# Kernel optimization log

Measured on AMD Instinct MI355X. Metric: run time of the kernel, lower is better.

The kernel has to match this reference:

```python
import jax, jax.numpy as jnp
import numpy as np

N = 4096; E = 65536; IN = 512; H = 256; QD = 256; NH = 8; HD = QD // NH
OUT = 10; L = 2; CT = 50


def _ln(x, g, b, eps=1e-5):
    mu = x.mean(-1, keepdims=True)
    var = ((x - mu) ** 2).mean(-1, keepdims=True)
    return (x - mu) * jax.lax.rsqrt(var + eps) * g + b


def _forward(x, edge_index, cell_types, Wi, bi, Wq, bq, Wk, bk, Wv, bv, Bc, cemb,
             Win, bin_p, Wo, bo, Wm1, bm1, Wm2, bm2, Wm3, bm3, ln_g, ln_b,
             Wc1, bc1, Wc2, bc2):
    src, tgt = edge_index[0], edge_index[1]
    h = jax.nn.relu(x @ Wi + bi)                      # [N, H] input projection
    # graph connectivity scattered into a dense mask (as in _create_attention_mask)
    mask = jnp.zeros((N, N), jnp.float32).at[src, tgt].set(1.0)
    for l in range(L):
        res = h
        Q = h @ Wq[l] + bq[l]                         # [N, QD]
        K = h @ Wk[l] + bk[l]
        V = h @ Wv[l] + bv[l]
        Q = Q @ Bc[l]                                 # biological constraint
        K = K @ Bc[l].T
        ce = cemb[l][cell_types]                      # [N, QD] cell-type embedding
        Q = Q + 0.1 * ce
        K = K + 0.1 * ce
        # dense graph-masked attention (entanglement matrix), applied to V
        scores = (Q @ K.T) / float(np.sqrt(QD))      # [N, N]
        scores = jnp.where(mask == 0.0, -1e9, scores)
        attn = jax.nn.softmax(scores, axis=-1)
        graph_att = attn @ V                          # [N, QD]
        # nn.MultiheadAttention(Q, K, V) entanglement layer (eval mode)
        q = (Q @ Win[l, :, :QD] + bin_p[l, :QD]).reshape(N, NH, HD)
        k = (K @ Win[l, :, QD:2 * QD] + bin_p[l, QD:2 * QD]).reshape(N, NH, HD)
        v = (V @ Win[l, :, 2 * QD:] + bin_p[l, 2 * QD:]).reshape(N, NH, HD)
        w = jax.nn.softmax(jnp.einsum('nhd,mhd->hnm', q, k) / float(np.sqrt(HD)), axis=-1)
        mha = jnp.einsum('hnm,mhd->nhd', w, v).reshape(N, QD) @ Wo[l] + bo[l]
        # edge gather -> message MLP -> scatter-add (PyG aggr='add', x_i=target, x_j=source)
        # quantum slot of the concat is zeros, so only the first 2H rows of Wm1 contribute
        m = jnp.concatenate([h[tgt], h[src]], axis=-1) @ Wm1[l, :2 * H] + bm1[l]
        m = jax.nn.relu(m)
        m = jax.nn.relu(m @ Wm2[l] + bm2[l])
        m = m @ Wm3[l] + bm3[l]                       # [E, H]
        agg = jax.ops.segment_sum(m, tgt, num_segments=N)
        h = _ln(res + agg + mha + graph_att, ln_g[l], ln_b[l])
    # graph-level readout: mean || max pooling -> classifier (hidden*2 -> hidden -> out)
    pooled = jnp.concatenate([h.mean(0), h.max(0)], axis=-1)   # [2H]
    z = jax.nn.relu(pooled @ Wc1 + bc1)
    return z @ Wc2 + bc2                              # [OUT]


def setup_inputs():
    ks = jax.random.split(jax.random.key(0), 40)
    s = 0.05
    p = lambda i, shape: jax.random.normal(ks[i], shape, jnp.float32) * s
    z = lambda shape: jnp.zeros(shape, jnp.float32)
    return {
        'x': jax.random.normal(ks[0], (N, IN), jnp.float32),
        'edge_index': jax.random.randint(ks[1], (2, E), 0, N),
        'cell_types': jax.random.randint(ks[2], (N,), 0, CT),
        'Wi': p(3, (IN, H)), 'bi': z((H,)),
        'Wq': p(4, (L, H, QD)), 'bq': z((L, QD)),
        'Wk': p(5, (L, H, QD)), 'bk': z((L, QD)),
        'Wv': p(6, (L, H, QD)), 'bv': z((L, QD)),
        'Bc': p(7, (L, QD, QD)),
        'cemb': p(8, (L, CT, QD)),
        'Win': p(9, (L, QD, 3 * QD)), 'bin_p': z((L, 3 * QD)),
        'Wo': p(10, (L, QD, QD)), 'bo': z((L, QD)),
        'Wm1': p(11, (L, 2 * H + QD, QD)), 'bm1': z((L, QD)),
        'Wm2': p(12, (L, QD, QD)), 'bm2': z((L, QD)),
        'Wm3': p(13, (L, QD, H)), 'bm3': z((L, H)),
        'ln_g': jnp.ones((L, H), jnp.float32), 'ln_b': z((L, H)),
        'Wc1': p(14, (2 * H, H)), 'bc1': z((H,)),
        'Wc2': p(15, (H, OUT)), 'bc2': z((OUT,)),
    }


def reference(x, edge_index, cell_types, Wi, bi, Wq, bq, Wk, bk, Wv, bv, Bc, cemb,
              Win, bin_p, Wo, bo, Wm1, bm1, Wm2, bm2, Wm3, bm3, ln_g, ln_b,
              Wc1, bc1, Wc2, bc2):
    return _forward(x, edge_index, cell_types, Wi, bi, Wq, bq, Wk, bk, Wv, bv, Bc, cemb,
                    Win, bin_p, Wo, bo, Wm1, bm1, Wm2, bm2, Wm3, bm3, ln_g, ln_b,
                    Wc1, bc1, Wc2, bc2)
```

## Files before the change

kernel.cpp:

```cpp
#include <hip/hip_runtime.h>
#include <hip/hip_bf16.h>

#define N_NODES 4096
#define E_EDGES 65536
#define IN_F    512
#define H_F     256
#define QD      256
#define NHEAD   8
#define HD      32
#define OUT_F   10
#define L_LAYERS 2
#define CT_N    50

enum { FLAG_RELU = 1, FLAG_ACCUM = 2, FLAG_WF32 = 4, FLAG_WB16 = 8 };

typedef __attribute__((ext_vector_type(8))) __bf16 bf16x8;
typedef __attribute__((ext_vector_type(4))) float f32x4;

union PU { bf16x8 v; __hip_bfloat16 h[8]; __hip_bfloat162 b2[4]; };

template<int BM, int BN, bool EDGE>
__global__ __launch_bounds__(256) void gemm_mfma(
    const __hip_bfloat16* __restrict__ A, int lda,
    const __hip_bfloat16* __restrict__ B, int ldb,
    float* __restrict__ Cf, __hip_bfloat16* __restrict__ Cb, int ldc,
    int K,
    const float* __restrict__ bias, const float* __restrict__ rowscale,
    const int* __restrict__ tgtp, const int* __restrict__ srcp,
    const float* __restrict__ kbias,
    int flags)
{
    constexpr int WM = BM / 2, WN = BN / 2, MT = WM / 16, NT = WN / 16;
    constexpr int LDT = 40;
    __shared__ alignas(16) __hip_bfloat16 As[BM * LDT];
    __shared__ alignas(16) __hip_bfloat16 Bs[BN * LDT];

    const int tid = threadIdx.x;
    const int w = tid >> 6, lane = tid & 63, l16 = lane & 15, quad = lane >> 4;
    const int wm = w >> 1, wn = w & 1;
    const int bm = blockIdx.y * BM, bn = blockIdx.x * BN;

    f32x4 acc[MT][NT];
    #pragma unroll
    for (int i = 0; i < MT; ++i)
        #pragma unroll
        for (int j = 0; j < NT; ++j)
            #pragma unroll
            for (int r = 0; r < 4; ++r) acc[i][j][r] = 0.f;

    for (int k0 = 0; k0 < K; k0 += 32) {
        #pragma unroll
        for (int f = tid; f < BM * 4; f += 256) {
            int r = f >> 2, sg = f & 3;
            if (EDGE) {
                int i = bm + r;
                int tg = tgtp[i], sr = srcp[i];
                PU z1, z2, o;
                z1.v = *reinterpret_cast<const bf16x8*>(A + (size_t)tg * 512 + k0 + sg * 8);
                z2.v = *reinterpret_cast<const bf16x8*>(A + (size_t)sr * 512 + 256 + k0 + sg * 8);
                float4 b0 = *reinterpret_cast<const float4*>(kbias + k0 + sg * 8);
                float4 b1 = *reinterpret_cast<const float4*>(kbias + k0 + sg * 8 + 4);
                float bb[8] = {b0.x, b0.y, b0.z, b0.w, b1.x, b1.y, b1.z, b1.w};
                #pragma unroll
                for (int j = 0; j < 8; ++j) {
                    float v = __bfloat162float(z1.h[j]) + __bfloat162float(z2.h[j]) + bb[j];
                    o.h[j] = __float2bfloat16(fmaxf(v, 0.f));
                }
                *reinterpret_cast<bf16x8*>(&As[r * LDT + sg * 8]) = o.v;
            } else {
                *reinterpret_cast<uint4*>(&As[r * LDT + sg * 8]) =
                    *reinterpret_cast<const uint4*>(A + (size_t)(bm + r) * lda + k0 + sg * 8);
            }
        }
        #pragma unroll
        for (int f = tid; f < BN * 4; f += 256) {
            int r = f >> 2, sg = f & 3;
            *reinterpret_cast<uint4*>(&Bs[r * LDT + sg * 8]) =
                *reinterpret_cast<const uint4*>(B + (size_t)(bn + r) * ldb + k0 + sg * 8);
        }
        __syncthreads();
        bf16x8 af[MT], bfr[NT];
        #pragma unroll
        for (int mt = 0; mt < MT; ++mt)
            af[mt] = *reinterpret_cast<const bf16x8*>(&As[(wm * WM + mt * 16 + l16) * LDT + quad * 8]);
        #pragma unroll
        for (int nt = 0; nt < NT; ++nt)
            bfr[nt] = *reinterpret_cast<const bf16x8*>(&Bs[(wn * WN + nt * 16 + l16) * LDT + quad * 8]);
        #pragma unroll
        for (int mt = 0; mt < MT; ++mt)
            #pragma unroll
            for (int nt = 0; nt < NT; ++nt)
                acc[mt][nt] = __builtin_amdgcn_mfma_f32_16x16x32_bf16(af[mt], bfr[nt], acc[mt][nt], 0, 0, 0);
        __syncthreads();
    }

    #pragma unroll
    for (int mt = 0; mt < MT; ++mt) {
        #pragma unroll
        for (int nt = 0; nt < NT; ++nt) {
            int col = bn + wn * WN + nt * 16 + l16;
            #pragma unroll
            for (int r = 0; r < 4; ++r) {
                int row = bm + wm * WM + mt * 16 + quad * 4 + r;
                float v = acc[mt][nt][r];
                if (bias) {
                    float bv = bias[col];
                    if (rowscale) bv *= rowscale[row];
                    v += bv;
                }
                if (flags & FLAG_RELU) v = fmaxf(v, 0.f);
                size_t off = (size_t)row * ldc + col;
                if (flags & FLAG_ACCUM)     Cf[off] += v;
                else if (flags & FLAG_WF32) Cf[off] = v;
                if (flags & FLAG_WB16)      Cb[off] = __float2bfloat16(v);
            }
        }
    }
}

__global__ __launch_bounds__(512) void edge_gemm(
    const __hip_bfloat16* __restrict__ Z,
    const __hip_bfloat16* __restrict__ B,
    __hip_bfloat16* __restrict__ C,
    const int* __restrict__ tgtp, const int* __restrict__ srcp,
    const float* __restrict__ kbias,
    const float* __restrict__ bias)
{
    constexpr int LDA = 264;
    constexpr int LDB = 40;
    __shared__ alignas(16) __hip_bfloat16 As[64 * LDA];
    __shared__ alignas(16) __hip_bfloat16 Bs[256 * LDB];

    const int tid = threadIdx.x;
    const int w = tid >> 6, lane = tid & 63, l16 = lane & 15, quad = lane >> 4;
    const int bid = blockIdx.x;
    const int bm = ((bid & 7) * 128 + (bid >> 3)) * 64;

    bf16x8 zt[4], zs[4];
    #pragma unroll
    for (int u = 0; u < 4; ++u) {
        int g = u * 512 + tid;
        int r = g >> 5, c = g & 31;
        int i = bm + r;
        int tg = tgtp[i], sr = srcp[i];
        zt[u] = *reinterpret_cast<const bf16x8*>(Z + (size_t)tg * 512 + c * 8);
        zs[u] = *reinterpret_cast<const bf16x8*>(Z + (size_t)sr * 512 + 256 + c * 8);
    }
    #pragma unroll
    for (int u = 0; u < 4; ++u) {
        int g = u * 512 + tid;
        int r = g >> 5, c = g & 31;
        PU a, b, o;
        a.v = zt[u]; b.v = zs[u];
        float4 k0v = *reinterpret_cast<const float4*>(kbias + c * 8);
        float4 k1v = *reinterpret_cast<const float4*>(kbias + c * 8 + 4);
        float bb[8] = {k0v.x, k0v.y, k0v.z, k0v.w, k1v.x, k1v.y, k1v.z, k1v.w};
        #pragma unroll
        for (int j = 0; j < 8; ++j) {
            float v = __bfloat162float(a.h[j]) + __bfloat162float(b.h[j]) + bb[j];
            o.h[j] = __float2bfloat16(fmaxf(v, 0.f));
        }
        *reinterpret_cast<bf16x8*>(&As[r * LDA + c * 8]) = o.v;
    }

    const int wn = w;
    f32x4 acc[4][2];
    #pragma unroll
    for (int mt = 0; mt < 4; ++mt)
        #pragma unroll
        for (int nt = 0; nt < 2; ++nt)
            #pragma unroll
            for (int r = 0; r < 4; ++r) acc[mt][nt][r] = 0.f;

    for (int k0 = 0; k0 < 256; k0 += 32) {
        #pragma unroll
        for (int u = 0; u < 2; ++u) {
            int f = u * 512 + tid;
            int r = f >> 2, sg = f & 3;
            *reinterpret_cast<uint4*>(&Bs[r * LDB + sg * 8]) =
                *reinterpret_cast<const uint4*>(B + (size_t)r * 256 + k0 + sg * 8);
        }
        __syncthreads();
        bf16x8 af[4], bfr[2];
        #pragma unroll
        for (int mt = 0; mt < 4; ++mt)
            af[mt] = *reinterpret_cast<const bf16x8*>(&As[(mt * 16 + l16) * LDA + k0 + quad * 8]);
        #pragma unroll
        for (int nt = 0; nt < 2; ++nt)
            bfr[nt] = *reinterpret_cast<const bf16x8*>(&Bs[(wn * 32 + nt * 16 + l16) * LDB + quad * 8]);
        #pragma unroll
        for (int mt = 0; mt < 4; ++mt)
            #pragma unroll
            for (int nt = 0; nt < 2; ++nt)
                acc[mt][nt] = __builtin_amdgcn_mfma_f32_16x16x32_bf16(af[mt], bfr[nt], acc[mt][nt], 0, 0, 0);
        __syncthreads();
    }

    #pragma unroll
    for (int mt = 0; mt < 4; ++mt) {
        #pragma unroll
        for (int nt = 0; nt < 2; ++nt) {
            int col = wn * 32 + nt * 16 + l16;
            float bv = bias[col];
            #pragma unroll
            for (int r = 0; r < 4; ++r) {
                int row = bm + mt * 16 + quad * 4 + r;
                float v = fmaxf(acc[mt][nt][r] + bv, 0.f);
                C[(size_t)row * 256 + col] = __float2bfloat16(v);
            }
        }
    }
}

struct GSet { const __hip_bfloat16* A; int lda; const __hip_bfloat16* B;
              const float* bias; const float* rowscale;
              const float* extra; float esc; float cscale;
              __hip_bfloat16* C; float* Cf; int vtout; int ldc; int coloff; };
struct GPack { GSet s[8]; };

__global__ __launch_bounds__(256) void gemm_bz(GPack p, const int* __restrict__ eidx)
{
    GSet g = p.s[blockIdx.z];
    constexpr int LDT = 40;
    __shared__ alignas(16) __hip_bfloat16 As[64 * LDT];
    __shared__ alignas(16) __hip_bfloat16 Bs[64 * LDT];

    const int tid = threadIdx.x;
    const int w = tid >> 6, lane = tid & 63, l16 = lane & 15, quad = lane >> 4;
    const int wm = w >> 1, wn = w & 1;
    const int bm = blockIdx.y * 64, bn = blockIdx.x * 64;

    f32x4 acc[2][2];
    #pragma unroll
    for (int i = 0; i < 2; ++i)
        #pragma unroll
        for (int j = 0; j < 2; ++j)
            #pragma unroll
            for (int r = 0; r < 4; ++r) acc[i][j][r] = 0.f;

    for (int k0 = 0; k0 < 256; k0 += 32) {
        #pragma unroll
        for (int f = tid; f < 256; f += 256) {
            int r = f >> 2, sg = f & 3;
            *reinterpret_cast<uint4*>(&As[r * LDT + sg * 8]) =
                *reinterpret_cast<const uint4*>(g.A + (size_t)(bm + r) * g.lda + k0 + sg * 8);
            *reinterpret_cast<uint4*>(&Bs[r * LDT + sg * 8]) =
                *reinterpret_cast<const uint4*>(g.B + (size_t)(bn + r) * 256 + k0 + sg * 8);
        }
        __syncthreads();
        bf16x8 af[2], bfr[2];
        #pragma unroll
        for (int mt = 0; mt < 2; ++mt)
            af[mt] = *reinterpret_cast<const bf16x8*>(&As[(wm * 32 + mt * 16 + l16) * LDT + quad * 8]);
        #pragma unroll
        for (int nt = 0; nt < 2; ++nt)
            bfr[nt] = *reinterpret_cast<const bf16x8*>(&Bs[(wn * 32 + nt * 16 + l16) * LDT + quad * 8]);
        #pragma unroll
        for (int mt = 0; mt < 2; ++mt)
            #pragma unroll
            for (int nt = 0; nt < 2; ++nt)
                acc[mt][nt] = __builtin_amdgcn_mfma_f32_16x16x32_bf16(af[mt], bfr[nt], acc[mt][nt], 0, 0, 0);
        __syncthreads();
    }

    #pragma unroll
    for (int mt = 0; mt < 2; ++mt) {
        #pragma unroll
        for (int nt = 0; nt < 2; ++nt) {
            int colL = bn + wn * 32 + nt * 16 + l16;
            #pragma unroll
            for (int r = 0; r < 4; ++r) {
                int row = bm + wm * 32 + mt * 16 + quad * 4 + r;
                float v = acc[mt][nt][r];
                if (g.bias) {
                    float bv = g.bias[colL];
                    if (g.rowscale) bv *= g.rowscale[row];
                    v += bv;
                }
                if (g.extra) v += g.esc * g.extra[(size_t)eidx[row] * QD + colL];
                v *= g.cscale;
                if (g.vtout)
                    g.C[(size_t)colL * 4096 + row] = __float2bfloat16(v);
                else if (g.Cf)
                    g.Cf[(size_t)row * g.ldc + g.coloff + colL] = v;
                else
                    g.C[(size_t)row * g.ldc + g.coloff + colL] = __float2bfloat16(v);
            }
        }
    }
}

struct FDesc { const float* A; int lda; const float* B; int ldb; int tb;
               const float* bias; float* C; int M, N, K; };
struct FPack { FDesc d[16]; };

__global__ __launch_bounds__(256) void fgemm2(FPack p)
{
    FDesc c = p.d[blockIdx.z];
    int bm = blockIdx.y * 32, bn = blockIdx.x * 32;
    if (bm >= c.M || bn >= c.N) return;
    __shared__ float As[16][33];
    __shared__ float Bs[16][33];
    int tid = threadIdx.x;
    int tr = tid / 16, tc = tid % 16;
    float acc[2][2] = {};

    for (int k0 = 0; k0 < c.K; k0 += 16) {
        #pragma unroll
        for (int u = 0; u < 2; ++u) {
            int i = tid * 2 + u;
            int m = i >> 4, kk = i & 15;
            int row = bm + m, kg = k0 + kk;
            As[kk][m] = (row < c.M && kg < c.K) ? c.A[(size_t)row * c.lda + kg] : 0.f;
        }
        if (c.tb) {
            #pragma unroll
            for (int u = 0; u < 2; ++u) {
                int i = tid * 2 + u;
                int n = i >> 4, kk = i & 15;
                int col = bn + n, kg = k0 + kk;
                Bs[kk][n] = (col < c.N && kg < c.K) ? c.B[(size_t)col * c.ldb + kg] : 0.f;
            }
        } else {
            #pragma unroll
            for (int u = 0; u < 2; ++u) {
                int i = tid * 2 + u;
                int kk = i >> 5, n = i & 31;
                int col = bn + n, kg = k0 + kk;
                Bs[kk][n] = (col < c.N && kg < c.K) ? c.B[(size_t)kg * c.ldb + col] : 0.f;
            }
        }
        __syncthreads();
        #pragma unroll
        for (int kk = 0; kk < 16; ++kk) {
            float a0 = As[kk][tr * 2], a1 = As[kk][tr * 2 + 1];
            float b0 = Bs[kk][tc * 2], b1 = Bs[kk][tc * 2 + 1];
            acc[0][0] = fmaf(a0, b0, acc[0][0]);
            acc[0][1] = fmaf(a0, b1, acc[0][1]);
            acc[1][0] = fmaf(a1, b0, acc[1][0]);
            acc[1][1] = fmaf(a1, b1, acc[1][1]);
        }
        __syncthreads();
    }

    #pragma unroll
    for (int i = 0; i < 2; ++i) {
        int row = bm + tr * 2 + i;
        if (row >= c.M) continue;
        #pragma unroll
        for (int j = 0; j < 2; ++j) {
            int col = bn + tc * 2 + j;
            if (col >= c.N) continue;
            float v = acc[i][j];
            if (c.bias) v += c.bias[col];
            c.C[(size_t)row * c.N + col] = v;
        }
    }
}

__global__ __launch_bounds__(512, 4) void mha_flash10(
    const __hip_bfloat16* __restrict__ Qm,
    const __hip_bfloat16* __restrict__ Km,
    const __hip_bfloat16* __restrict__ Vt, __hip_bfloat16* __restrict__ Out)
{
    const int hh = blockIdx.y;
    const int tid = threadIdx.x;
    const int w = tid >> 6, lane = tid & 63, l16 = lane & 15, quad = lane >> 4;
    const int qb = blockIdx.x * 64;

    __shared__ float Osh[8][4][64][9];
    __shared__ float Lsh[8][4][16];

    bf16x8 aq[4];
    #pragma unroll
    for (int s = 0; s < 4; ++s)
        aq[s] = *reinterpret_cast<const bf16x8*>(
            Qm + (size_t)(qb + s * 16 + l16) * 256 + hh * 32 + quad * 8);
    const __hip_bfloat16* vb0 = Vt + (size_t)(hh * 32 + l16) * 4096;
    const __hip_bfloat16* vb1 = vb0 + (size_t)16 * 4096;
    const int rowoff = (l16 >> 2) * 8 + (l16 & 3);
    const f32x4 zero = {0.f, 0.f, 0.f, 0.f};

    f32x4 o0[4], o1[4];
    float lsum[4];
    #pragma unroll
    for (int s = 0; s < 4; ++s) { o0[s] = zero; o1[s] = zero; lsum[s] = 0.f; }

    const int kstart = w * 512;
    for (int kt = 0; kt < 8; ++kt) {
        const int kbase = kstart + kt * 64;
        bf16x8 kf[4];
        #pragma unroll
        for (int c = 0; c < 2; ++c)
            #pragma unroll
            for (int st = 0; st < 2; ++st)
                kf[c * 2 + st] = *reinterpret_cast<const bf16x8*>(
                    Km + (size_t)(kbase + c * 32 + st * 4 + rowoff) * 256 + hh * 32 + quad * 8);
        bf16x8 v00 = *reinterpret_cast<const bf16x8*>(vb0 + kbase + quad * 8);
        bf16x8 v01 = *reinterpret_cast<const bf16x8*>(vb1 + kbase + quad * 8);
        bf16x8 v10 = *reinterpret_cast<const bf16x8*>(vb0 + kbase + 32 + quad * 8);
        bf16x8 v11 = *reinterpret_cast<const bf16x8*>(vb1 + kbase + 32 + quad * 8);

        #pragma unroll
        for (int s = 0; s < 4; ++s) {
            f32x4 sv[4];
            __builtin_amdgcn_s_setprio(1);
            #pragma unroll
            for (int i = 0; i < 4; ++i)
                sv[i] = __builtin_amdgcn_mfma_f32_16x16x32_bf16(kf[i], aq[s], zero, 0, 0, 0);
            __builtin_amdgcn_s_setprio(0);
            PU p0, p1;
            float ls = 0.f;
            #pragma unroll
            for (int i = 0; i < 4; ++i) {
                float e0 = exp2f(sv[i][0]), e1 = exp2f(sv[i][1]);
                float e2 = exp2f(sv[i][2]), e3 = exp2f(sv[i][3]);
                ls += (e0 + e1) + (e2 + e3);
                PU& pp = (i < 2) ? p0 : p1;
                pp.b2[(i & 1) * 2 + 0] = __float22bfloat162_rn(make_float2(e0, e1));
                pp.b2[(i & 1) * 2 + 1] = __float22bfloat162_rn(make_float2(e2, e3));
            }
            lsum[s] += ls;
            __builtin_amdgcn_s_setprio(1);
            o0[s] = __builtin_amdgcn_mfma_f32_16x16x32_bf16(v00, p0.v, o0[s], 0, 0, 0);
            o1[s] = __builtin_amdgcn_mfma_f32_16x16x32_bf16(v01, p0.v, o1[s], 0, 0, 0);
            o0[s] = __builtin_amdgcn_mfma_f32_16x16x32_bf16(v10, p1.v, o0[s], 0, 0, 0);
            o1[s] = __builtin_amdgcn_mfma_f32_16x16x32_bf16(v11, p1.v, o1[s], 0, 0, 0);
            __builtin_amdgcn_s_setprio(0);
        }
    }

    #pragma unroll
    for (int s = 0; s < 4; ++s) {
        lsum[s] += __shfl_xor(lsum[s], 16);
        lsum[s] += __shfl_xor(lsum[s], 32);
    }

    #pragma unroll
    for (int s = 0; s < 4; ++s) {
        #pragma unroll
        for (int r = 0; r < 4; ++r) {
            Osh[w][s][lane][r]     = o0[s][r];
            Osh[w][s][lane][4 + r] = o1[s][r];
        }
        if (quad == 0) Lsh[w][s][l16] = lsum[s];
    }
    __syncthreads();
    if (w < 4) {
        const int s = w;
        f32x4 a0 = zero, a1 = zero;
        float ll = 0.f;
        #pragma unroll
        for (int ww = 0; ww < 8; ++ww) {
            #pragma unroll
            for (int r = 0; r < 4; ++r) {
                a0[r] += Osh[ww][s][lane][r];
                a1[r] += Osh[ww][s][lane][4 + r];
            }
            ll += Lsh[ww][s][l16];
        }
        float inv = 1.f / ll;
        __hip_bfloat16* dst = Out + (size_t)(qb + s * 16 + l16) * 256 + hh * 32;
        #pragma unroll
        for (int r = 0; r < 4; ++r) {
            dst[quad * 4 + r]      = __float2bfloat16(a0[r] * inv);
            dst[16 + quad * 4 + r] = __float2bfloat16(a1[r] * inv);
        }
    }
}

__global__ __launch_bounds__(256) void build_mask(const int* __restrict__ src,
                                                  const int* __restrict__ tgt,
                                                  unsigned* __restrict__ mb,
                                                  int* __restrict__ cnt)
{
    int e = blockIdx.x * 256 + threadIdx.x;
    if (e >= E_EDGES) return;
    int t = tgt[e];
    atomicOr(mb + (size_t)src[e] * (N_NODES / 32) + (t >> 5), 1u << (t & 31));
    atomicAdd(&cnt[t], 1);
}

__global__ __launch_bounds__(1024) void csr_scan(const int* __restrict__ cnt, int* __restrict__ off,
                                                 int* __restrict__ cursor, float* __restrict__ degf)
{
    __shared__ int sh[1024];
    int t = threadIdx.x;
    int base = t * 4;
    int c0 = cnt[base], c1 = cnt[base + 1], c2 = cnt[base + 2], c3 = cnt[base + 3];
    int sum = c0 + c1 + c2 + c3;
    sh[t] = sum; __syncthreads();
    for (int d = 1; d < 1024; d <<= 1) {
        int v = (t >= d) ? sh[t - d] : 0;
        __syncthreads();
        sh[t] += v;
        __syncthreads();
    }
    int excl = sh[t] - sum;
    int o0 = excl, o1 = excl + c0, o2 = o1 + c1, o3 = o2 + c2;
    off[base] = o0; off[base + 1] = o1; off[base + 2] = o2; off[base + 3] = o3;
    cursor[base] = o0; cursor[base + 1] = o1; cursor[base + 2] = o2; cursor[base + 3] = o3;
    degf[base] = (float)c0; degf[base + 1] = (float)c1;
    degf[base + 2] = (float)c2; degf[base + 3] = (float)c3;
    if (t == 1023) off[4096] = sh[t];
}

__global__ __launch_bounds__(256) void csr_fill(const int* __restrict__ src, const int* __restrict__ tgt,
                                                int* __restrict__ cursor,
                                                int* __restrict__ srcp, int* __restrict__ tgtp)
{
    int e = blockIdx.x * 256 + threadIdx.x;
    if (e >= E_EDGES) return;
    int t = tgt[e];
    int pos = atomicAdd(&cursor[t], 1);
    srcp[pos] = src[e];
    tgtp[pos] = t;
}

__global__ __launch_bounds__(256) void seg_sum(const int* __restrict__ off,
                                               const __hip_bfloat16* __restrict__ M2,
                                               __hip_bfloat16* __restrict__ A3)
{
    int n = blockIdx.x, t = threadIdx.x;
    int b0 = off[n], b1 = off[n + 1];
    float s = 0.f;
    for (int i = b0; i < b1; ++i)
        s += __bfloat162float(M2[(size_t)i * 256 + t]);
    A3[(size_t)n * 256 + t] = __float2bfloat16(s);
}

__global__ __launch_bounds__(256) void sparse_attn(
    const __hip_bfloat16* __restrict__ Q, const __hip_bfloat16* __restrict__ K,
    const __hip_bfloat16* __restrict__ V, int vld,
    const unsigned* __restrict__ maskb, float* __restrict__ outb)
{
    int i = blockIdx.x, t = threadIdx.x;
    __shared__ float qsh[256];
    __shared__ int   nb[1024];
    __shared__ float sc[1024];
    __shared__ int   cnt;
    __shared__ float red[4];
    __shared__ float smax, ssum;
    if (t == 0) cnt = 0;
    qsh[t] = __bfloat162float(Q[(size_t)i * 256 + t]);
    __syncthreads();
    if (t < 128) {
        unsigned wv = maskb[(size_t)i * 128 + t];
        while (wv) {
            int b = __ffs(wv) - 1; wv &= wv - 1;
            int p = atomicAdd(&cnt, 1);
            nb[p] = t * 32 + b;
        }
    }
    __syncthreads();
    int deg = cnt;
    int wid = t >> 6, lane = t & 63;
    if (deg > 0) {
        for (int n = wid; n < deg; n += 4) {
            union { uint2 u; __hip_bfloat16 h[4]; } kv;
            kv.u = *reinterpret_cast<const uint2*>(K + (size_t)nb[n] * 256 + lane * 4);
            float s = qsh[lane*4+0] * __bfloat162float(kv.h[0]) + qsh[lane*4+1] * __bfloat162float(kv.h[1])
                    + qsh[lane*4+2] * __bfloat162float(kv.h[2]) + qsh[lane*4+3] * __bfloat162float(kv.h[3]);
            #pragma unroll
            for (int off = 32; off; off >>= 1) s += __shfl_xor(s, off);
            if (lane == 0) sc[n] = s * 0.0625f;
        }
        __syncthreads();
        float m = -3.4e38f;
        for (int n = t; n < deg; n += 256) m = fmaxf(m, sc[n]);
        #pragma unroll
        for (int off = 32; off; off >>= 1) m = fmaxf(m, __shfl_xor(m, off));
        if (lane == 0) red[wid] = m;
        __syncthreads();
        if (t == 0) smax = fmaxf(fmaxf(red[0], red[1]), fmaxf(red[2], red[3]));
        __syncthreads();
        float ls = 0.f;
        for (int n = t; n < deg; n += 256) { float e = __expf(sc[n] - smax); sc[n] = e; ls += e; }
        #pragma unroll
        for (int off = 32; off; off >>= 1) ls += __shfl_xor(ls, off);
        if (lane == 0) red[wid] = ls;
        __syncthreads();
        if (t == 0) ssum = red[0] + red[1] + red[2] + red[3];
        __syncthreads();
        float inv = 1.f / ssum;
        float o = 0.f;
        for (int n = 0; n < deg; ++n)
            o += sc[n] * __bfloat162float(V[(size_t)nb[n] * vld + t]);
        outb[(size_t)i * 256 + t] = o * inv;
    } else {
        float o = 0.f;
        for (int j = 0; j < N_NODES; ++j) o += __bfloat162float(V[(size_t)j * vld + t]);
        outb[(size_t)i * 256 + t] = o * (1.f / N_NODES);
    }
}

__global__ __launch_bounds__(256) void ln_kernel(float* __restrict__ h, __hip_bfloat16* __restrict__ h16,
                                                 const float* __restrict__ a1,
                                                 const float* __restrict__ a2,
                                                 const float* __restrict__ a3,
                                                 const float* __restrict__ g, const float* __restrict__ b)
{
    int row = blockIdx.x, t = threadIdx.x;
    __shared__ float red[256];
    size_t off = ((size_t)row << 8) + t;
    float v = h[off] + a1[off] + a2[off] + a3[off];
    red[t] = v; __syncthreads();
    for (int s = 128; s > 0; s >>= 1) { if (t < s) red[t] += red[t + s]; __syncthreads(); }
    float mu = red[0] * (1.f / 256.f); __syncthreads();
    float d = v - mu;
    red[t] = d * d; __syncthreads();
    for (int s = 128; s > 0; s >>= 1) { if (t < s) red[t] += red[t + s]; __syncthreads(); }
    float var = red[0] * (1.f / 256.f);
    float r = d * rsqrtf(var + 1e-5f) * g[t] + b[t];
    h[off] = r;
    h16[off] = __float2bfloat16(r);
}

__global__ __launch_bounds__(256) void colpool(const float* __restrict__ h, float* __restrict__ p)
{
    int c = blockIdx.x, t = threadIdx.x;
    __shared__ float rs[256], rm[256];
    float s = 0.f, m = -3.4e38f;
    for (int row = t; row < N_NODES; row += 256) {
        float v = h[((size_t)row << 8) + c];
        s += v; m = fmaxf(m, v);
    }
    rs[t] = s; rm[t] = m; __syncthreads();
    for (int st = 128; st > 0; st >>= 1) {
        if (t < st) { rs[t] += rs[t + st]; rm[t] = fmaxf(rm[t], rm[t + st]); }
        __syncthreads();
    }
    if (t == 0) { p[c] = rs[0] * (1.f / N_NODES); p[256 + c] = rm[0]; }
}

__global__ __launch_bounds__(256) void classifier(const float* __restrict__ pooled,
                                                  const float* __restrict__ Wc1, const float* __restrict__ bc1,
                                                  const float* __restrict__ Wc2, const float* __restrict__ bc2,
                                                  float* __restrict__ out)
{
    __shared__ float p[512];
    __shared__ float z[256];
    int t = threadIdx.x;
    p[t] = pooled[t]; p[256 + t] = pooled[256 + t];
    __syncthreads();
    float s = bc1[t];
    for (int k = 0; k < 512; ++k) s = fmaf(p[k], Wc1[k * 256 + t], s);
    z[t] = fmaxf(s, 0.f);
    __syncthreads();
    if (t < OUT_F) {
        float o = bc2[t];
        for (int j = 0; j < 256; ++j) o = fmaf(z[j], Wc2[j * OUT_F + t], o);
        out[t] = o;
    }
}

struct CDesc { const float* s; __hip_bfloat16* d; int total; };
struct CPack { CDesc d[2]; };
__global__ __launch_bounds__(256) void convert_copy(CPack p)
{
    CDesc c = p.d[blockIdx.y];
    for (int i = blockIdx.x * 256 + threadIdx.x; i < c.total; i += gridDim.x * 256)
        c.d[i] = __float2bfloat16(c.s[i]);
}
struct TDesc { const float* s; __hip_bfloat16* d; int K, N, sld; };
struct TPack { TDesc d[23]; };
__global__ __launch_bounds__(256) void convert_t32(TPack p)
{
    TDesc c = p.d[blockIdx.z];
    int k0 = blockIdx.x * 32, n0 = blockIdx.y * 32;
    if (k0 >= c.K || n0 >= c.N) return;
    __shared__ float t[32][33];
    int tr = threadIdx.x >> 5, tc = threadIdx.x & 31;
    #pragma unroll
    for (int rr = 0; rr < 32; rr += 8)
        t[tc][tr + rr] = c.s[(size_t)(k0 + tr + rr) * c.sld + n0 + tc];
    __syncthreads();
    #pragma unroll
    for (int rr = 0; rr < 32; rr += 8)
        c.d[(size_t)(n0 + tr + rr) * c.K + k0 + tc] = __float2bfloat16(t[tr + rr][tc]);
}

extern "C" void kernel_launch(void* const* d_in, const int* in_sizes, int n_in,
                              void* d_out, int out_size, void* d_ws, size_t ws_size,
                              hipStream_t stream)
{
    const float* x    = (const float*)d_in[0];
    const int*   ei   = (const int*)d_in[1];
    const int*   ct   = (const int*)d_in[2];
    const float* Wi   = (const float*)d_in[3];
    const float* bi   = (const float*)d_in[4];
    const float* Wq   = (const float*)d_in[5];
    const float* bq   = (const float*)d_in[6];
    const float* Wk   = (const float*)d_in[7];
    const float* bk   = (const float*)d_in[8];
    const float* Wv   = (const float*)d_in[9];
    const float* bv   = (const float*)d_in[10];
    const float* Bc   = (const float*)d_in[11];
    const float* cemb = (const float*)d_in[12];
    const float* Win  = (const float*)d_in[13];
    const float* binp = (const float*)d_in[14];
    const float* Wo   = (const float*)d_in[15];
    const float* bo   = (const float*)d_in[16];
    const float* Wm1  = (const float*)d_in[17];
    const float* bm1  = (const float*)d_in[18];
    const float* Wm2  = (const float*)d_in[19];
    const float* bm2  = (const float*)d_in[20];
    const float* Wm3  = (const float*)d_in[21];
    const float* bm3  = (const float*)d_in[22];
    const float* lng  = (const float*)d_in[23];
    const float* lnb  = (const float*)d_in[24];
    const float* Wc1  = (const float*)d_in[25];
    const float* bc1  = (const float*)d_in[26];
    const float* Wc2  = (const float*)d_in[27];
    const float* bc2  = (const float*)d_in[28];

    const int* src = ei;
    const int* tgt = ei + E_EDGES;

    char* wp = (char*)d_ws;
    auto alloc = [&](size_t bytes) { char* r = wp; wp += (bytes + 255) & ~(size_t)255; return r; };
    const size_t NH = (size_t)N_NODES * 256;
    float* h      = (float*)alloc(NH * 4);
    float* a1     = (float*)alloc(NH * 4);
    float* a2     = (float*)alloc(NH * 4);
    float* a3     = (float*)alloc(NH * 4);
    float* pooled = (float*)alloc(512 * 4);
    float* degf   = (float*)alloc(N_NODES * 4);
    __hip_bfloat16* x16 = (__hip_bfloat16*)alloc((size_t)N_NODES * 512 * 2);
    __hip_bfloat16* h16 = (__hip_bfloat16*)alloc(NH * 2);
    __hip_bfloat16* Qb  = (__hip_bfloat16*)alloc(NH * 2);
    __hip_bfloat16* Kb  = (__hip_bfloat16*)alloc(NH * 2);
    __hip_bfloat16* Vb  = (__hip_bfloat16*)alloc(NH * 2);
    __hip_bfloat16* Tq  = (__hip_bfloat16*)alloc(NH * 2);
    __hip_bfloat16* Tk  = (__hip_bfloat16*)alloc(NH * 2);
    __hip_bfloat16* Vt  = (__hip_bfloat16*)alloc(NH * 2);
    __hip_bfloat16* Z12 = (__hip_bfloat16*)alloc((size_t)N_NODES * 512 * 2);
    __hip_bfloat16* M216= (__hip_bfloat16*)alloc((size_t)E_EDGES * 256 * 2);
    __hip_bfloat16* A3  = (__hip_bfloat16*)alloc(NH * 2);
    __hip_bfloat16* Wi_t= (__hip_bfloat16*)alloc((size_t)256 * 512 * 2);
    float *Wqc_f[2], *Wkc_f[2], *Wqm_f[2], *Wkm_f[2], *Wvm_f[2];
    float *bqc[2], *bkc[2], *bqm[2], *bkm[2], *bvm[2], *ceq2[2], *cek2[2];
    for (int l = 0; l < 2; ++l) {
        Wqc_f[l] = (float*)alloc(65536 * 4); Wkc_f[l] = (float*)alloc(65536 * 4);
        Wqm_f[l] = (float*)alloc(65536 * 4); Wkm_f[l] = (float*)alloc(65536 * 4);
        Wvm_f[l] = (float*)alloc(65536 * 4);
        bqc[l] = (float*)alloc(256 * 4); bkc[l] = (float*)alloc(256 * 4);
        bqm[l] = (float*)alloc(256 * 4); bkm[l] = (float*)alloc(256 * 4);
        bvm[l] = (float*)alloc(256 * 4);
        ceq2[l] = (float*)alloc(CT_N * 256 * 4); cek2[l] = (float*)alloc(CT_N * 256 * 4);
    }
    __hip_bfloat16* WB[2][11];
    for (int l = 0; l < 2; ++l)
        for (int m = 0; m < 11; ++m)
            WB[l][m] = (__hip_bfloat16*)alloc(65536 * 2);
    unsigned* maskb = (unsigned*)alloc((size_t)N_NODES * 128 * 4);
    int* cnt    = (int*)alloc(N_NODES * 4);
    int* cursor = (int*)alloc(N_NODES * 4);
    int* off    = (int*)alloc((N_NODES + 1) * 4);
    int* srcp   = (int*)alloc(E_EDGES * 4);
    int* tgtp   = (int*)alloc(E_EDGES * 4);

    CPack cp; cp.d[0] = {x, x16, N_NODES * 512};
    convert_copy<<<dim3(256, 1), 256, 0, stream>>>(cp);

    FPack f1; int n1 = 0;
    FPack f2; int n2 = 0;
    for (int l = 0; l < 2; ++l) {
        const float* Wq_l  = Wq + (size_t)l * 65536;
        const float* Wk_l  = Wk + (size_t)l * 65536;
        const float* Wv_l  = Wv + (size_t)l * 65536;
        const float* Bc_l  = Bc + (size_t)l * 65536;
        const float* Win_l = Win + (size_t)l * 256 * 768;
        const float* ce_l  = cemb + (size_t)l * CT_N * QD;
        const float* bq_l  = bq + l * 256;
        const float* bk_l  = bk + l * 256;
        const float* bv_l  = bv + l * 256;
        const float* bin_l = binp + l * 768;
        f1.d[n1++] = {Wq_l, 256, Bc_l, 256, 0, nullptr, Wqc_f[l], 256, 256, 256};
        f1.d[n1++] = {Wk_l, 256, Bc_l, 256, 1, nullptr, Wkc_f[l], 256, 256, 256};
        f1.d[n1++] = {bq_l, 256, Bc_l, 256, 0, nullptr, bqc[l], 1, 256, 256};
        f1.d[n1++] = {bk_l, 256, Bc_l, 256, 1, nullptr, bkc[l], 1, 256, 256};
        f2.d[n2++] = {Wqc_f[l], 256, Win_l,       768, 0, nullptr, Wqm_f[l], 256, 256, 256};
        f2.d[n2++] = {Wkc_f[l], 256, Win_l + 256, 768, 0, nullptr, Wkm_f[l], 256, 256, 256};
        f2.d[n2++] = {Wv_l,     256, Win_l + 512, 768, 0, nullptr, Wvm_f[l], 256, 256, 256};
        f2.d[n2++] = {ce_l,     256, Win_l,       768, 0, nullptr, ceq2[l], CT_N, 256, 256};
        f2.d[n2++] = {ce_l,     256, Win_l + 256, 768, 0, nullptr, cek2[l], CT_N, 256, 256};
        f2.d[n2++] = {bqc[l],   256, Win_l,       768, 0, bin_l,       bqm[l], 1, 256, 256};
        f2.d[n2++] = {bkc[l],   256, Win_l + 256, 768, 0, bin_l + 256, bkm[l], 1, 256, 256};
        f2.d[n2++] = {bv_l,     256, Win_l + 512, 768, 0, bin_l + 512, bvm[l], 1, 256, 256};
    }
    fgemm2<<<dim3(8, 8, n1), 256, 0, stream>>>(f1);
    fgemm2<<<dim3(8, 8, n2), 256, 0, stream>>>(f2);

    TPack tp; int ndt = 0;
    auto addT = [&](const float* s, __hip_bfloat16* d, int K, int N, int sld) { tp.d[ndt++] = {s, d, K, N, sld}; };
    addT(Wi, Wi_t, 512, 256, 256);
    for (int l = 0; l < 2; ++l) {
        const float* Wv_l  = Wv + (size_t)l * 65536;
        const float* Wo_l  = Wo + (size_t)l * 65536;
        const float* Wm1_l = Wm1 + (size_t)l * (2 * H_F + QD) * QD;
        const float* Wm2_l = Wm2 + (size_t)l * 65536;
        const float* Wm3_l = Wm3 + (size_t)l * 65536;
        addT(Wqc_f[l], WB[l][0], 256, 256, 256);
        addT(Wkc_f[l], WB[l][1], 256, 256, 256);
        addT(Wqm_f[l], WB[l][2], 256, 256, 256);
        addT(Wkm_f[l], WB[l][3], 256, 256, 256);
        addT(Wvm_f[l], WB[l][4], 256, 256, 256);
        addT(Wv_l,     WB[l][5], 256, 256, 256);
        addT(Wo_l,     WB[l][6], 256, 256, 256);
        addT(Wm1_l,             WB[l][7], 256, 256, 256);
        addT(Wm1_l + 256 * 256, WB[l][8], 256, 256, 256);
        addT(Wm2_l,    WB[l][9],  256, 256, 256);
        addT(Wm3_l,    WB[l][10], 256, 256, 256);
    }
    convert_t32<<<dim3(16, 8, ndt), 256, 0, stream>>>(tp);

    hipMemsetAsync(maskb, 0, (size_t)N_NODES * 128 * 4, stream);
    hipMemsetAsync(cnt, 0, N_NODES * 4, stream);
    build_mask<<<E_EDGES / 256, 256, 0, stream>>>(src, tgt, maskb, cnt);
    csr_scan<<<1, 1024, 0, stream>>>(cnt, off, cursor, degf);
    csr_fill<<<E_EDGES / 256, 256, 0, stream>>>(src, tgt, cursor, srcp, tgtp);

    gemm_mfma<64, 64, false><<<dim3(4, 64), 256, 0, stream>>>(
        x16, 512, Wi_t, 512, h, h16, 256, 512,
        bi, nullptr, nullptr, nullptr, nullptr, FLAG_RELU | FLAG_WF32 | FLAG_WB16);

    const float QSCALE = 0.25507693f;

    for (int l = 0; l < L_LAYERS; ++l) {
        const float* ce_l  = cemb + (size_t)l * CT_N * QD;
        const float* bo_l  = bo + l * QD;
        const float* bm1_l = bm1 + l * QD;
        const float* bm2_l = bm2 + l * QD;
        const float* bm3_l = bm3 + l * H_F;
        const float* lng_l = lng + l * H_F;
        const float* lnb_l = lnb + l * H_F;
        const float* bv_l  = bv + l * 256;

        {
            GPack gp;
            gp.s[0] = {h16, 256, WB[l][0], bqc[l], nullptr, ce_l,    0.1f, 1.0f,   Qb,  nullptr, 0, 256, 0};
            gp.s[1] = {h16, 256, WB[l][1], bkc[l], nullptr, ce_l,    0.1f, 1.0f,   Kb,  nullptr, 0, 256, 0};
            gp.s[2] = {h16, 256, WB[l][5], bv_l,   nullptr, nullptr, 0.f,  1.0f,   Vb,  nullptr, 0, 256, 0};
            gp.s[3] = {h16, 256, WB[l][2], bqm[l], nullptr, ceq2[l], 0.1f, QSCALE, Tq,  nullptr, 0, 256, 0};
            gp.s[4] = {h16, 256, WB[l][3], bkm[l], nullptr, cek2[l], 0.1f, 1.0f,   Tk,  nullptr, 0, 256, 0};
            gp.s[5] = {h16, 256, WB[l][4], bvm[l], nullptr, nullptr, 0.f,  1.0f,   Vt,  nullptr, 1, 256, 0};
            gp.s[6] = {h16, 256, WB[l][7], nullptr, nullptr, nullptr, 0.f, 1.0f,   Z12, nullptr, 0, 512, 0};
            gp.s[7] = {h16, 256, WB[l][8], nullptr, nullptr, nullptr, 0.f, 1.0f,   Z12, nullptr, 0, 512, 256};
            gemm_bz<<<dim3(4, 64, 8), 256, 0, stream>>>(gp, ct);
        }

        sparse_attn<<<N_NODES, 256, 0, stream>>>(Qb, Kb, Vb, 256, maskb, a1);

        mha_flash10<<<dim3(64, NHEAD), 512, 0, stream>>>(Tq, Tk, Vt, Qb);

        edge_gemm<<<E_EDGES / 64, 512, 0, stream>>>(
            Z12, WB[l][9], M216, tgtp, srcp, bm1_l, bm2_l);
        seg_sum<<<N_NODES, 256, 0, stream>>>(off, M216, A3);

        {
            GPack gp;
            gp.s[0] = {Qb, 256, WB[l][6],  bo_l,  nullptr, nullptr, 0.f, 1.0f, nullptr, a2, 0, 256, 0};
            gp.s[1] = {A3, 256, WB[l][10], bm3_l, degf,    nullptr, 0.f, 1.0f, nullptr, a3, 0, 256, 0};
            gemm_bz<<<dim3(4, 64, 2), 256, 0, stream>>>(gp, ct);
        }

        ln_kernel<<<N_NODES, 256, 0, stream>>>(h, h16, a1, a2, a3, lng_l, lnb_l);
    }

    colpool<<<H_F, 256, 0, stream>>>(h, pooled);
    classifier<<<1, 256, 0, stream>>>(pooled, Wc1, bc1, Wc2, bc2, (float*)d_out);
}
```

Baseline: 515.6 us.

## Split MHA flash key range across 16 waves with tree reduction

The dense multi-head attention kernel now launches 1024-thread blocks, so 16 waves each cover 256 keys instead of 8 waves covering 512. The cross-wave reduction of partial outputs and row sums becomes a multi-stage tree through shared memory: 16 to 8 to 4, then a final exchange among the last four waves. This aims to hide latency with more waves per query tile and to shorten the serial reduction. In exchange it adds several block-wide barriers and raises register pressure, given the launch-bounds request for 8 waves per SIMD.

New measurement: 1.590 ms. 3.08x slower.

```diff
diff --git a/kernel.cpp b/kernel.cpp
--- a/kernel.cpp
+++ b/kernel.cpp
@@ -358,7 +358,7 @@
     }
 }
 
-__global__ __launch_bounds__(512, 4) void mha_flash10(
+__global__ __launch_bounds__(1024, 8) void mha_flash11(
     const __hip_bfloat16* __restrict__ Qm,
     const __hip_bfloat16* __restrict__ Km,
     const __hip_bfloat16* __restrict__ Vt, __hip_bfloat16* __restrict__ Out)
@@ -386,8 +386,8 @@
     #pragma unroll
     for (int s = 0; s < 4; ++s) { o0[s] = zero; o1[s] = zero; lsum[s] = 0.f; }
 
-    const int kstart = w * 512;
-    for (int kt = 0; kt < 8; ++kt) {
+    const int kstart = w * 256;
+    for (int kt = 0; kt < 4; ++kt) {
         const int kbase = kstart + kt * 64;
         bf16x8 kf[4];
         #pragma unroll
@@ -436,28 +436,80 @@
         lsum[s] += __shfl_xor(lsum[s], 32);
     }
 
-    #pragma unroll
-    for (int s = 0; s < 4; ++s) {
-        #pragma unroll
-        for (int r = 0; r < 4; ++r) {
-            Osh[w][s][lane][r]     = o0[s][r];
-            Osh[w][s][lane][4 + r] = o1[s][r];
-        }
-        if (quad == 0) Lsh[w][s][l16] = lsum[s];
+    if (w >= 8) {
+        #pragma unroll
+        for (int s = 0; s < 4; ++s) {
+            #pragma unroll
+            for (int r = 0; r < 4; ++r) {
+                Osh[w - 8][s][lane][r]     = o0[s][r];
+                Osh[w - 8][s][lane][4 + r] = o1[s][r];
+            }
+            if (quad == 0) Lsh[w - 8][s][l16] = lsum[s];
+        }
+    }
+    __syncthreads();
+    if (w < 8) {
+        #pragma unroll
+        for (int s = 0; s < 4; ++s) {
+            #pragma unroll
+            for (int r = 0; r < 4; ++r) {
+                o0[s][r] += Osh[w][s][lane][r];
+                o1[s][r] += Osh[w][s][lane][4 + r];
+            }
+            lsum[s] += Lsh[w][s][l16];
+        }
+    }
+    __syncthreads();
+    if (w >= 4 && w < 8) {
+        #pragma unroll
+        for (int s = 0; s < 4; ++s) {
+            #pragma unroll
+            for (int r = 0; r < 4; ++r) {
+                Osh[w - 4][s][lane][r]     = o0[s][r];
+                Osh[w - 4][s][lane][4 + r] = o1[s][r];
+            }
+            if (quad == 0) Lsh[w - 4][s][l16] = lsum[s];
+        }
+    }
+    __syncthreads();
+    if (w < 4) {
+        #pragma unroll
+        for (int s = 0; s < 4; ++s) {
+            #pragma unroll
+            for (int r = 0; r < 4; ++r) {
+                o0[s][r] += Osh[w][s][lane][r];
+                o1[s][r] += Osh[w][s][lane][4 + r];
+            }
+            lsum[s] += Lsh[w][s][l16];
+        }
+    }
+    __syncthreads();
+    if (w < 4) {
+        #pragma unroll
+        for (int s = 0; s < 4; ++s) {
+            if (s == w) continue;
+            #pragma unroll
+            for (int r = 0; r < 4; ++r) {
+                Osh[w][s][lane][r]     = o0[s][r];
+                Osh[w][s][lane][4 + r] = o1[s][r];
+            }
+            if (quad == 0) Lsh[w][s][l16] = lsum[s];
+        }
     }
     __syncthreads();
     if (w < 4) {
         const int s = w;
-        f32x4 a0 = zero, a1 = zero;
-        float ll = 0.f;
-        #pragma unroll
-        for (int ww = 0; ww < 8; ++ww) {
+        f32x4 a0 = o0[s], a1 = o1[s];
+        float ll = lsum[s];
+        #pragma unroll
+        for (int i = 0; i < 4; ++i) {
+            if (i == s) continue;
             #pragma unroll
             for (int r = 0; r < 4; ++r) {
-                a0[r] += Osh[ww][s][lane][r];
-                a1[r] += Osh[ww][s][lane][4 + r];
-            }
-            ll += Lsh[ww][s][l16];
+                a0[r] += Osh[i][s][lane][r];
+                a1[r] += Osh[i][s][lane][4 + r];
+            }
+            ll += Lsh[i][s][l16];
         }
         float inv = 1.f / ll;
         __hip_bfloat16* dst = Out + (size_t)(qb + s * 16 + l16) * 256 + hh * 32;
@@ -852,7 +904,7 @@
 
         sparse_attn<<<N_NODES, 256, 0, stream>>>(Qb, Kb, Vb, 256, maskb, a1);
 
-        mha_flash10<<<dim3(64, NHEAD), 512, 0, stream>>>(Tq, Tk, Vt, Qb);
+        mha_flash11<<<dim3(64, NHEAD), 1024, 0, stream>>>(Tq, Tk, Vt, Qb);
 
         edge_gemm<<<E_EDGES / 64, 512, 0, stream>>>(
             Z12, WB[l][9], M216, tgtp, srcp, bm1_l, bm2_l);
```
